# Performance work log

Measured on AMD Instinct MI355X. Metric: run time of the kernel, lower is better.

The kernel has to match this reference:

```python
import jax, jax.numpy as jnp
import numpy as np

DIM = 2048
N_HEADS = 16
Q_RANK = 1536
KV_RANK = 512
D_NOPE = 128
D_ROPE = 64
D_V = 128
EPS = 1e-6
B, S = 2, 2048
ROPE_THETA = 10000.0


def rmsnorm(x, w, eps=EPS):
    return x * jax.lax.rsqrt(jnp.mean(x * x, axis=-1, keepdims=True) + eps) * w


def apply_rope(x):
    # x: [b, h, s, d] with d even; LLaMA-style interleaved pair rotation
    b, h, s, d = x.shape
    inv_freq = 1.0 / (ROPE_THETA ** (jnp.arange(0, d, 2, dtype=jnp.float32) / d))
    ang = jnp.arange(s, dtype=jnp.float32)[:, None] * inv_freq[None, :]  # [s, d/2]
    cos, sin = jnp.cos(ang), jnp.sin(ang)
    xr = x.reshape(b, h, s, d // 2, 2)
    x1, x2 = xr[..., 0], xr[..., 1]
    o1 = x1 * cos - x2 * sin
    o2 = x1 * sin + x2 * cos
    return jnp.stack([o1, o2], axis=-1).reshape(b, h, s, d)


def setup_inputs() -> dict:
    key = jax.random.key(0)
    ks = jax.random.split(key, 10)
    std = 0.02
    return {
        "x": jax.random.normal(ks[0], (B, S, DIM), dtype=jnp.float32),
        "wq_down": jax.random.normal(ks[1], (Q_RANK, DIM), dtype=jnp.float32) * std,
        "q_norm_w": jnp.ones((Q_RANK,), dtype=jnp.float32),
        "wq_up": jax.random.normal(ks[2], (N_HEADS * D_NOPE, Q_RANK), dtype=jnp.float32) * std,
        "wq_rope": jax.random.normal(ks[3], (N_HEADS * D_ROPE, Q_RANK), dtype=jnp.float32) * std,
        "wkv_down": jax.random.normal(ks[4], (KV_RANK, DIM), dtype=jnp.float32) * std,
        "kv_norm_w": jnp.ones((KV_RANK,), dtype=jnp.float32),
        "wkv_up": jax.random.normal(ks[5], (N_HEADS * (D_NOPE + D_V), KV_RANK), dtype=jnp.float32) * std,
        "wk_rope": jax.random.normal(ks[6], (D_ROPE, DIM), dtype=jnp.float32) * std,
        "wo": jax.random.normal(ks[7], (DIM, N_HEADS * D_V), dtype=jnp.float32) * std,
    }


def reference(x, wq_down, q_norm_w, wq_up, wq_rope, wkv_down, kv_norm_w, wkv_up, wk_rope, wo):
    bs, s, _ = x.shape
    # low-rank Q path
    q_c = rmsnorm(x @ wq_down.T, q_norm_w)                              # [b,s,qr]
    q_nope = (q_c @ wq_up.T).reshape(bs, s, N_HEADS, D_NOPE).transpose(0, 2, 1, 3)
    q_pe = (q_c @ wq_rope.T).reshape(bs, s, N_HEADS, D_ROPE).transpose(0, 2, 1, 3)
    # low-rank KV path
    kv_c = rmsnorm(x @ wkv_down.T, kv_norm_w)                           # [b,s,kvr]
    kv_up = (kv_c @ wkv_up.T).reshape(bs, s, N_HEADS, D_NOPE + D_V)
    k_nope = kv_up[..., :D_NOPE].transpose(0, 2, 1, 3)                  # [b,h,s,dn]
    v = kv_up[..., D_NOPE:].transpose(0, 2, 1, 3)                       # [b,h,s,dv]
    # shared rope key (1 head), broadcast across heads
    k_rope = (x @ wk_rope.T).reshape(bs, s, 1, D_ROPE).transpose(0, 2, 1, 3)  # [b,1,s,dr]
    q_pe = apply_rope(q_pe)
    k_rope = apply_rope(k_rope)
    q = jnp.concatenate([q_nope, q_pe], axis=-1)                        # [b,h,s,dn+dr]
    k = jnp.concatenate([k_nope, jnp.broadcast_to(k_rope, (bs, N_HEADS, s, D_ROPE))], axis=-1)
    scale = 1.0 / np.sqrt(D_NOPE + D_ROPE)
    scores = jnp.einsum('bhqd,bhkd->bhqk', q, k) * scale                # [b,h,s,s]
    causal = jnp.tril(jnp.ones((s, s), dtype=bool))
    scores = jnp.where(causal, scores, -jnp.inf)
    probs = jax.nn.softmax(scores, axis=-1)
    out = jnp.einsum('bhqk,bhkv->bhqv', probs, v)                       # [b,h,s,dv]
    out = out.transpose(0, 2, 1, 3).reshape(bs, s, N_HEADS * D_V)
    return out @ wo.T
```

## Files before the change

### kernel.cpp

```cpp
#include <hip/hip_runtime.h>
#include <stdint.h>

typedef _Float16 f16x8 __attribute__((ext_vector_type(8)));
typedef _Float16 f16x4 __attribute__((ext_vector_type(4)));
typedef float fx4 __attribute__((ext_vector_type(4)));

static constexpr int S_LEN = 2048;
static constexpr int BATCH = 2;
static constexpr int TOKENS = BATCH * S_LEN;
static constexpr int DIM = 2048;
static constexpr int NH = 16;
static constexpr int QR = 1536;
static constexpr int KVR = 512;
static constexpr int DN = 128;
static constexpr int DR = 64;
static constexpr int DV = 128;

__device__ __forceinline__ void async16(const _Float16* g, _Float16* lds_base_uniform) {
  __builtin_amdgcn_global_load_lds(
      (const __attribute__((address_space(1))) void*)g,
      (__attribute__((address_space(3))) void*)lds_base_uniform, 16, 0, 0);
}

#define ROR16(x, ctrl) \
  __uint_as_float(__builtin_amdgcn_update_dpp(__float_as_uint(x), __float_as_uint(x), \
                                              (ctrl), 0xF, 0xF, false))

struct CvtSegs {
  const float* src[8];
  _Float16* dst[8];
  int n4[8];
  int cum[9];
};
__global__ __launch_bounds__(256) void cvt_all(CvtSegs s) {
  const int b = blockIdx.x;
  int seg = 0;
#pragma unroll
  for (int k = 0; k < 7; ++k) seg += (b >= s.cum[seg + 1]) ? 1 : 0;
  const int i = (b - s.cum[seg]) * 256 + threadIdx.x;
  if (i >= s.n4[seg]) return;
  fx4 v = *(const fx4*)(s.src[seg] + (size_t)i * 4);
  f16x4 o;
  o[0] = (_Float16)v[0]; o[1] = (_Float16)v[1];
  o[2] = (_Float16)v[2]; o[3] = (_Float16)v[3];
  *(f16x4*)(s.dst[seg] + (size_t)i * 4) = o;
}

template <int MODE>
__global__ __launch_bounds__(256) void gemm_nt(const _Float16* __restrict__ A,
                                               const _Float16* __restrict__ W,
                                               void* __restrict__ C0v,
                                               void* __restrict__ C1v,
                                               int M, int N, int K) {
  __shared__ __attribute__((aligned(16))) _Float16 As[2][128 * 32];
  __shared__ __attribute__((aligned(16))) _Float16 Ws[2][128 * 32];
  const int tid = threadIdx.x;
  const int lane = tid & 63;
  const int wave = tid >> 6;
  const int wr = (wave >> 1) * 64;
  const int wc = (wave & 1) * 64;
  const int m16 = lane & 15;
  const int quad = lane >> 4;
  const int m0 = blockIdx.y * 128;
  const int n0 = blockIdx.x * 128;

  auto stage = [&](int buf, int k0) {
#pragma unroll
    for (int p = 0; p < 2; ++p) {
      const int cb = p * 256 + wave * 64;
      const int ch = cb + lane;
      const int r = ch >> 2;
      const int c8 = (ch & 3) * 8;
      async16(A + (size_t)(m0 + r) * K + k0 + c8, &As[buf][cb * 8]);
      async16(W + (size_t)(n0 + r) * K + k0 + c8, &Ws[buf][cb * 8]);
    }
  };

  const fx4 fz = {0.f, 0.f, 0.f, 0.f};
  fx4 acc[4][4];
#pragma unroll
  for (int i = 0; i < 4; ++i)
#pragma unroll
    for (int j = 0; j < 4; ++j) acc[i][j] = fz;

  const int nkt = K >> 5;
  stage(0, 0);
  for (int kt = 0; kt < nkt; ++kt) {
    __syncthreads();
    if (kt + 1 < nkt) stage((kt + 1) & 1, (kt + 1) * 32);
    const _Float16* as = As[kt & 1];
    const _Float16* ws = Ws[kt & 1];
    f16x8 af[4], wf[4];
#pragma unroll
    for (int i = 0; i < 4; ++i)
      af[i] = *(const f16x8*)(&as[(wr + i * 16 + m16) * 32 + quad * 8]);
#pragma unroll
    for (int j = 0; j < 4; ++j)
      wf[j] = *(const f16x8*)(&ws[(wc + j * 16 + m16) * 32 + quad * 8]);
#pragma unroll
    for (int i = 0; i < 4; ++i)
#pragma unroll
      for (int j = 0; j < 4; ++j)
        acc[i][j] = __builtin_amdgcn_mfma_f32_16x16x32_f16(af[i], wf[j], acc[i][j], 0, 0, 0);
  }

#pragma unroll
  for (int j = 0; j < 4; ++j) {
    const int col = n0 + wc + j * 16 + m16;
    if (MODE == 2) {
      _Float16* KN = (_Float16*)C0v;
      _Float16* VT = (_Float16*)C1v;
      const int head = col >> 8;
      const int sub = col & 255;
      if (sub < 128) {
#pragma unroll
        for (int i = 0; i < 4; ++i)
#pragma unroll
          for (int r = 0; r < 4; ++r)
            KN[(size_t)(m0 + wr + i * 16 + quad * 4 + r) * 2048 + head * 128 + sub] =
                (_Float16)acc[i][j][r];
      } else {
        const int dv = sub - 128;
#pragma unroll
        for (int i = 0; i < 4; ++i) {
          f16x4 v;
#pragma unroll
          for (int r = 0; r < 4; ++r) v[r] = (_Float16)acc[i][j][r];
          *(f16x4*)(&VT[(size_t)(head * 128 + dv) * TOKENS + m0 + wr + i * 16 + quad * 4]) = v;
        }
      }
    } else if (MODE == 3) {
#pragma unroll
      for (int i = 0; i < 4; ++i)
#pragma unroll
        for (int r = 0; r < 4; ++r) {
          const size_t row = (size_t)(m0 + wr + i * 16 + quad * 4 + r);
          if (col < 2048) ((_Float16*)C0v)[row * 2048 + col] = (_Float16)acc[i][j][r];
          else ((_Float16*)C1v)[row * 1024 + col - 2048] = (_Float16)acc[i][j][r];
        }
    } else if (MODE == 4) {
      if (col < 576) {
#pragma unroll
        for (int i = 0; i < 4; ++i)
#pragma unroll
          for (int r = 0; r < 4; ++r) {
            const size_t row = (size_t)(m0 + wr + i * 16 + quad * 4 + r);
            if (col < 512) ((_Float16*)C0v)[row * 512 + col] = (_Float16)acc[i][j][r];
            else ((_Float16*)C1v)[row * 64 + col - 512] = (_Float16)acc[i][j][r];
          }
      }
    } else {
      if (col < N) {
#pragma unroll
        for (int i = 0; i < 4; ++i)
#pragma unroll
          for (int r = 0; r < 4; ++r) {
            const size_t row = (size_t)(m0 + wr + i * 16 + quad * 4 + r);
            if (MODE == 0) ((_Float16*)C0v)[row * N + col] = (_Float16)acc[i][j][r];
            else ((float*)C0v)[row * N + col] = acc[i][j][r];
          }
      }
    }
  }
}

template <int NC>
__global__ __launch_bounds__(256) void rmsnorm_ip(_Float16* __restrict__ xx,
                                                  const float* __restrict__ w) {
  const int row = blockIdx.x;
  _Float16* p = xx + (size_t)row * NC;
  float ss = 0.f;
  for (int c = threadIdx.x; c < NC; c += 256) {
    const float v = (float)p[c];
    ss += v * v;
  }
#pragma unroll
  for (int d = 1; d < 64; d <<= 1) ss += __shfl_xor(ss, d);
  __shared__ float red[4];
  if ((threadIdx.x & 63) == 0) red[threadIdx.x >> 6] = ss;
  __syncthreads();
  const float rs = rsqrtf((red[0] + red[1] + red[2] + red[3]) * (1.0f / NC) + 1e-6f);
  for (int c = threadIdx.x; c < NC; c += 256)
    p[c] = (_Float16)((float)p[c] * rs * w[c]);
}

__global__ void rope_q(_Float16* __restrict__ qpe) {
  const int idx = blockIdx.x * 256 + threadIdx.x;
  const int t = idx >> 9;
  const int rem = idx & 511;
  const int hh = rem >> 5;
  const int i = rem & 31;
  const int s = t & (S_LEN - 1);
  const float fr = exp2f(-(float)i * 0.4152410118609203f);
  const float ang = (float)s * fr;
  const float sn = sinf(ang), cs = cosf(ang);
  const size_t base = (size_t)t * (NH * DR) + hh * DR + 2 * i;
  const float x1 = (float)qpe[base];
  const float x2 = (float)qpe[base + 1];
  qpe[base] = (_Float16)(x1 * cs - x2 * sn);
  qpe[base + 1] = (_Float16)(x1 * sn + x2 * cs);
}

__global__ void rope_k(_Float16* __restrict__ kr) {
  const int idx = blockIdx.x * 256 + threadIdx.x;
  const int t = idx >> 5;
  const int i = idx & 31;
  const int s = t & (S_LEN - 1);
  const float fr = exp2f(-(float)i * 0.4152410118609203f);
  const float ang = (float)s * fr;
  const float sn = sinf(ang), cs = cosf(ang);
  const size_t base = (size_t)t * DR + 2 * i;
  const float x1 = (float)kr[base];
  const float x2 = (float)kr[base + 1];
  kr[base] = (_Float16)(x1 * cs - x2 * sn);
  kr[base + 1] = (_Float16)(x1 * sn + x2 * cs);
}

__global__ __launch_bounds__(256, 2) void mla_attn(
    const _Float16* __restrict__ qn,
    const _Float16* __restrict__ qp,
    const _Float16* __restrict__ kn,
    const _Float16* __restrict__ kr,
    const _Float16* __restrict__ vT,
    _Float16* __restrict__ out)
{
  __shared__ __attribute__((aligned(16))) _Float16 Ks[2][768 * 8];
  __shared__ __attribute__((aligned(16))) _Float16 Vs[2][512 * 8];
  __shared__ __attribute__((aligned(16))) _Float16 Ps[4][16][40];

  const int bid = blockIdx.x;
  const int b = bid >> 8;
  const int u = bid & 255;
  const int h = u >> 4;
  const int jp = u & 15;
  const int tok0 = b * S_LEN;

  const int tid = threadIdx.x;
  const int lane = tid & 63;
  const int wave = tid >> 6;
  const int m16 = lane & 15;
  const int quad = lane >> 4;

  auto stageKV = [&](int buf, int kbase) {
#pragma unroll
    for (int j = 0; j < 3; ++j) {
      const int i = wave * 3 + j;
      const int ch = i * 2 + (lane >> 5);
      const int key = lane & 31;
      const _Float16* g = (ch < 16)
          ? kn + (size_t)(tok0 + kbase + key) * 2048 + h * 128 + ch * 8
          : kr + (size_t)(tok0 + kbase + key) * 64 + (ch - 16) * 8;
      async16(g, &Ks[buf][i * 512]);
    }
#pragma unroll
    for (int j = 0; j < 2; ++j) {
      const int i = wave * 2 + j;
      const int p = i * 64 + lane;
      const int dv = p >> 2;
      const int qc = p & 3;
      async16(vT + (size_t)(h * 128 + dv) * TOKENS + tok0 + kbase + qc * 8,
              &Vs[buf][i * 512]);
    }
  };

  const float scale2 = 0.07216878364870323f * 1.4426950408889634f;
  const fx4 fz = {0.f, 0.f, 0.f, 0.f};

  for (int half = 0; half < 2; ++half) {
    const int q32 = half ? (31 - jp) : jp;
    const int qb = q32 * 64;
    const int R0 = qb + wave * 16;

    f16x8 qf[6];
    {
      const size_t t = (size_t)(tok0 + qb + wave * 16 + m16);
#pragma unroll
      for (int kk = 0; kk < 4; ++kk)
        qf[kk] = *(const f16x8*)(qn + t * 2048 + h * 128 + kk * 32 + quad * 8);
#pragma unroll
      for (int kk = 0; kk < 2; ++kk)
        qf[4 + kk] = *(const f16x8*)(qp + t * 1024 + h * 64 + kk * 32 + quad * 8);
    }

    fx4 oacc[8];
#pragma unroll
    for (int n = 0; n < 8; ++n) oacc[n] = fz;
    float mst[4], lst[4];
#pragma unroll
    for (int r = 0; r < 4; ++r) { mst[r] = -3.0e38f; lst[r] = 0.f; }

    const int nkt = (qb >> 5) + 2;

    stageKV(0, 0);
    for (int kt = 0; kt < nkt; ++kt) {
      const int kbase = kt * 32;
      __syncthreads();
      if (kt + 1 < nkt) stageKV((kt + 1) & 1, kbase + 32);

      const bool live = (kbase <= R0 + 15);
      if (!live) continue;
      const _Float16* ks = Ks[kt & 1];
      const _Float16* vs = Vs[kt & 1];

      fx4 sc[2];
      sc[0] = fz; sc[1] = fz;
      __builtin_amdgcn_s_setprio(1);
#pragma unroll
      for (int kk = 0; kk < 6; ++kk) {
#pragma unroll
        for (int n = 0; n < 2; ++n) {
          f16x8 kf = *(const f16x8*)(&ks[(kk * 128 + quad * 32 + n * 16 + m16) * 8]);
          sc[n] = __builtin_amdgcn_mfma_f32_16x16x32_f16(qf[kk], kf, sc[n], 0, 0, 0);
        }
      }
      __builtin_amdgcn_s_setprio(0);

      f16x8 vf[8];
#pragma unroll
      for (int n8 = 0; n8 < 8; ++n8)
        vf[n8] = *(const f16x8*)(&vs[((n8 * 16 + m16) * 4 + quad) * 8]);

      const bool needmask = (kbase + 31 > R0);
      float alpha[4];
      bool any_upd = false;
#pragma unroll
      for (int r = 0; r < 4; ++r) {
        float v0 = sc[0][r] * scale2;
        float v1 = sc[1][r] * scale2;
        if (needmask) {
          const int qrow = R0 + quad * 4 + r;
          if (kbase + m16 > qrow)      v0 = -3.0e38f;
          if (kbase + 16 + m16 > qrow) v1 = -3.0e38f;
        }
        float mx = fmaxf(v0, v1);
        mx = fmaxf(mx, ROR16(mx, 0x128));
        mx = fmaxf(mx, ROR16(mx, 0x124));
        mx = fmaxf(mx, ROR16(mx, 0x122));
        mx = fmaxf(mx, ROR16(mx, 0x121));
        float al = 1.0f;
        if (__any(mx > mst[r] + 10.0f)) {
          const float mn = fmaxf(mst[r], mx);
          al = exp2f(mst[r] - mn);
          mst[r] = mn;
          any_upd = true;
        }
        alpha[r] = al;
        const float p0 = exp2f(v0 - mst[r]);
        const float p1 = exp2f(v1 - mst[r]);
        float ls = p0 + p1;
        ls += ROR16(ls, 0x128);
        ls += ROR16(ls, 0x124);
        ls += ROR16(ls, 0x122);
        ls += ROR16(ls, 0x121);
        lst[r] = lst[r] * al + ls;
        _Float16* pr = &Ps[wave][quad * 4 + r][0];
        pr[m16] = (_Float16)p0;
        pr[16 + m16] = (_Float16)p1;
      }
      if (any_upd) {
#pragma unroll
        for (int n8 = 0; n8 < 8; ++n8)
#pragma unroll
          for (int r = 0; r < 4; ++r) oacc[n8][r] *= alpha[r];
      }

      f16x8 pf = *(const f16x8*)(&Ps[wave][m16][quad * 8]);
      __builtin_amdgcn_s_setprio(1);
#pragma unroll
      for (int n8 = 0; n8 < 8; ++n8)
        oacc[n8] = __builtin_amdgcn_mfma_f32_16x16x32_f16(pf, vf[n8], oacc[n8], 0, 0, 0);
      __builtin_amdgcn_s_setprio(0);
    }

    float inv[4];
#pragma unroll
    for (int r = 0; r < 4; ++r) inv[r] = 1.0f / lst[r];
#pragma unroll
    for (int n8 = 0; n8 < 8; ++n8) {
#pragma unroll
      for (int r = 0; r < 4; ++r) {
        const size_t t = (size_t)(tok0 + qb + wave * 16 + quad * 4 + r);
        out[t * 2048 + h * 128 + n8 * 16 + m16] = (_Float16)(oacc[n8][r] * inv[r]);
      }
    }
  }
}

extern "C" void kernel_launch(void* const* d_in, const int* in_sizes, int n_in,
                              void* d_out, int out_size, void* d_ws, size_t ws_size,
                              hipStream_t stream) {
  const float* x         = (const float*)d_in[0];
  const float* wq_down   = (const float*)d_in[1];
  const float* q_norm_w  = (const float*)d_in[2];
  const float* wq_up     = (const float*)d_in[3];
  const float* wq_rope   = (const float*)d_in[4];
  const float* wkv_down  = (const float*)d_in[5];
  const float* kv_norm_w = (const float*)d_in[6];
  const float* wkv_up    = (const float*)d_in[7];
  const float* wk_rope   = (const float*)d_in[8];
  const float* wo        = (const float*)d_in[9];
  float* out = (float*)d_out;

  char* ws = (char*)d_ws;
  size_t off = 0;
  auto alloc = [&](size_t bytes) {
    char* p = ws + off;
    off += (bytes + 255) & ~(size_t)255;
    return p;
  };
  _Float16* x_h     = (_Float16*)alloc((size_t)TOKENS * DIM * 2);
  _Float16* wqd_h   = (_Float16*)alloc((size_t)QR * DIM * 2);
  _Float16* wquqr_h = (_Float16*)alloc((size_t)3072 * QR * 2);
  _Float16* wkvdr_h = (_Float16*)alloc((size_t)576 * DIM * 2);
  _Float16* wkvu_h  = (_Float16*)alloc((size_t)NH * 256 * KVR * 2);
  _Float16* wo_h    = (_Float16*)alloc((size_t)DIM * NH * DV * 2);
  _Float16* qc_h    = (_Float16*)alloc((size_t)TOKENS * QR * 2);
  _Float16* kvc_h   = (_Float16*)alloc((size_t)TOKENS * KVR * 2);
  _Float16* qnope_h = (_Float16*)alloc((size_t)TOKENS * 2048 * 2);
  _Float16* qpe_h   = (_Float16*)alloc((size_t)TOKENS * 1024 * 2);
  _Float16* knope_h = (_Float16*)alloc((size_t)TOKENS * 2048 * 2);
  _Float16* vT_h    = (_Float16*)alloc((size_t)2048 * TOKENS * 2);
  _Float16* krope_h = (_Float16*)alloc((size_t)TOKENS * DR * 2);
  _Float16* attn_h  = (_Float16*)alloc((size_t)TOKENS * 2048 * 2);

  CvtSegs cs;
  const float* srcs[8] = {x, wq_down, wq_up, wq_rope, wkv_down, wk_rope, wkv_up, wo};
  _Float16* dsts[8] = {x_h, wqd_h, wquqr_h, wquqr_h + (size_t)2048 * QR,
                       wkvdr_h, wkvdr_h + (size_t)512 * DIM, wkvu_h, wo_h};
  const size_t ns[8] = {(size_t)TOKENS * DIM, (size_t)QR * DIM, (size_t)2048 * QR,
                        (size_t)1024 * QR, (size_t)KVR * DIM, (size_t)DR * DIM,
                        (size_t)NH * 256 * KVR, (size_t)DIM * NH * DV};
  int cum = 0;
  for (int i = 0; i < 8; ++i) {
    cs.src[i] = srcs[i];
    cs.dst[i] = dsts[i];
    cs.n4[i] = (int)(ns[i] / 4);
    cs.cum[i] = cum;
    cum += (cs.n4[i] + 255) / 256;
  }
  cs.cum[8] = cum;
  cvt_all<<<dim3(cum), 256, 0, stream>>>(cs);

  auto gx = [](int n) { return (unsigned)((n + 127) / 128); };
  const unsigned gm = TOKENS / 128;

  gemm_nt<0><<<dim3(gx(QR), gm), 256, 0, stream>>>(x_h, wqd_h, qc_h, nullptr, TOKENS, QR, DIM);
  rmsnorm_ip<QR><<<dim3(TOKENS), 256, 0, stream>>>(qc_h, q_norm_w);
  gemm_nt<4><<<dim3(gx(576), gm), 256, 0, stream>>>(x_h, wkvdr_h, kvc_h, krope_h, TOKENS, 576, DIM);
  rmsnorm_ip<KVR><<<dim3(TOKENS), 256, 0, stream>>>(kvc_h, kv_norm_w);
  rope_k<<<dim3(TOKENS * 32 / 256), 256, 0, stream>>>(krope_h);
  gemm_nt<3><<<dim3(gx(3072), gm), 256, 0, stream>>>(qc_h, wquqr_h, qnope_h, qpe_h, TOKENS, 3072, QR);
  rope_q<<<dim3(TOKENS * NH * 32 / 256), 256, 0, stream>>>(qpe_h);
  gemm_nt<2><<<dim3(gx(4096), gm), 256, 0, stream>>>(kvc_h, wkvu_h, knope_h, vT_h, TOKENS, 4096, KVR);
  mla_attn<<<dim3(512), 256, 0, stream>>>(qnope_h, qpe_h, knope_h, krope_h, vT_h, attn_h);
  gemm_nt<1><<<dim3(gx(DIM), gm), 256, 0, stream>>>(attn_h, wo_h, out, nullptr, TOKENS, DIM, NH * DV);
}
```

Before: 529.2 us.

## Triple-buffer GEMM and attention LDS staging with explicit vmcnt waits; swizzle V tile

Moves both the GEMM and the attention kernel from double to triple LDS buffering. Loads are issued two tiles ahead, and the full __syncthreads is replaced by a partial s_waitcnt vmcnt plus a raw barrier, so global-to-LDS copies overlap more compute. The V tile in LDS is XOR-swizzled at both store and load to reduce bank conflicts. The extra buffers raise LDS use, which may lower occupancy in the attention kernel (launch bounds 256,2), and the hand-counted vmcnt values must match the number of async loads issued per stage.

```diff
diff --git a/kernel.cpp b/kernel.cpp
--- a/kernel.cpp
+++ b/kernel.cpp
@@ -22,6 +22,13 @@
       (__attribute__((address_space(3))) void*)lds_base_uniform, 16, 0, 0);
 }
 
+__device__ __forceinline__ void bar() {
+  asm volatile("" ::: "memory");
+  __builtin_amdgcn_s_barrier();
+  asm volatile("" ::: "memory");
+}
+#define VMWAIT(n) asm volatile("s_waitcnt vmcnt(" #n ")" ::: "memory")
+
 #define ROR16(x, ctrl) \
   __uint_as_float(__builtin_amdgcn_update_dpp(__float_as_uint(x), __float_as_uint(x), \
                                               (ctrl), 0xF, 0xF, false))
@@ -52,8 +59,8 @@
                                                void* __restrict__ C0v,
                                                void* __restrict__ C1v,
                                                int M, int N, int K) {
-  __shared__ __attribute__((aligned(16))) _Float16 As[2][128 * 32];
-  __shared__ __attribute__((aligned(16))) _Float16 Ws[2][128 * 32];
+  __shared__ __attribute__((aligned(16))) _Float16 As[3][128 * 32];
+  __shared__ __attribute__((aligned(16))) _Float16 Ws[3][128 * 32];
   const int tid = threadIdx.x;
   const int lane = tid & 63;
   const int wave = tid >> 6;
@@ -85,11 +92,17 @@
 
   const int nkt = K >> 5;
   stage(0, 0);
+  stage(1, 32);
+  int cur = 0;
   for (int kt = 0; kt < nkt; ++kt) {
-    __syncthreads();
-    if (kt + 1 < nkt) stage((kt + 1) & 1, (kt + 1) * 32);
-    const _Float16* as = As[kt & 1];
-    const _Float16* ws = Ws[kt & 1];
+    if (kt + 1 < nkt) { VMWAIT(4); } else { VMWAIT(0); }
+    bar();
+    if (kt + 2 < nkt) {
+      int b2 = cur + 2; if (b2 >= 3) b2 -= 3;
+      stage(b2, (kt + 2) * 32);
+    }
+    const _Float16* as = As[cur];
+    const _Float16* ws = Ws[cur];
     f16x8 af[4], wf[4];
 #pragma unroll
     for (int i = 0; i < 4; ++i)
@@ -102,6 +115,7 @@
 #pragma unroll
       for (int j = 0; j < 4; ++j)
         acc[i][j] = __builtin_amdgcn_mfma_f32_16x16x32_f16(af[i], wf[j], acc[i][j], 0, 0, 0);
+    if (++cur == 3) cur = 0;
   }
 
 #pragma unroll
@@ -224,8 +238,8 @@
     const _Float16* __restrict__ vT,
     _Float16* __restrict__ out)
 {
-  __shared__ __attribute__((aligned(16))) _Float16 Ks[2][768 * 8];
-  __shared__ __attribute__((aligned(16))) _Float16 Vs[2][512 * 8];
+  __shared__ __attribute__((aligned(16))) _Float16 Ks[3][768 * 8];
+  __shared__ __attribute__((aligned(16))) _Float16 Vs[3][512 * 8];
   __shared__ __attribute__((aligned(16))) _Float16 Ps[4][16][40];
 
   const int bid = blockIdx.x;
@@ -256,8 +270,9 @@
     for (int j = 0; j < 2; ++j) {
       const int i = wave * 2 + j;
       const int p = i * 64 + lane;
-      const int dv = p >> 2;
-      const int qc = p & 3;
+      const int L = p ^ ((p >> 3) & 3);
+      const int dv = L >> 2;
+      const int qc = L & 3;
       async16(vT + (size_t)(h * 128 + dv) * TOKENS + tok0 + kbase + qc * 8,
               &Vs[buf][i * 512]);
     }
@@ -291,16 +306,22 @@
 
     const int nkt = (qb >> 5) + 2;
 
+    bar();
     stageKV(0, 0);
+    stageKV(1, 32);
+    int cur = 0;
     for (int kt = 0; kt < nkt; ++kt) {
       const int kbase = kt * 32;
-      __syncthreads();
-      if (kt + 1 < nkt) stageKV((kt + 1) & 1, kbase + 32);
-
+      if (kt + 1 < nkt) { VMWAIT(5); } else { VMWAIT(0); }
+      bar();
+      if (kt + 2 < nkt) {
+        int b2 = cur + 2; if (b2 >= 3) b2 -= 3;
+        stageKV(b2, kbase + 64);
+      }
       const bool live = (kbase <= R0 + 15);
-      if (!live) continue;
-      const _Float16* ks = Ks[kt & 1];
-      const _Float16* vs = Vs[kt & 1];
+      if (!live) { if (++cur == 3) cur = 0; continue; }
+      const _Float16* ks = Ks[cur];
+      const _Float16* vs = Vs[cur];
 
       fx4 sc[2];
       sc[0] = fz; sc[1] = fz;
@@ -317,8 +338,10 @@
 
       f16x8 vf[8];
 #pragma unroll
-      for (int n8 = 0; n8 < 8; ++n8)
-        vf[n8] = *(const f16x8*)(&vs[((n8 * 16 + m16) * 4 + quad) * 8]);
+      for (int n8 = 0; n8 < 8; ++n8) {
+        const int c0 = (n8 * 16 + m16) * 4 + quad;
+        vf[n8] = *(const f16x8*)(&vs[(c0 ^ ((c0 >> 3) & 3)) * 8]);
+      }
 
       const bool needmask = (kbase + 31 > R0);
       float alpha[4];
@@ -370,6 +393,7 @@
       for (int n8 = 0; n8 < 8; ++n8)
         oacc[n8] = __builtin_amdgcn_mfma_f32_16x16x32_f16(pf, vf[n8], oacc[n8], 0, 0, 0);
       __builtin_amdgcn_s_setprio(0);
+      if (++cur == 3) cur = 0;
     }
 
     float inv[4];
```

After: 532.5 us. No clear change (+0.6%).
